# Kernel optimization log

Measured on AMD Instinct MI355X. Metric: run time of the kernel, lower is better.

Reference implementation:

```python
import jax, jax.numpy as jnp
import numpy as np

VEC_DIM = 128
NUM_DOCS = 1_000_000
NUM_WORDS = 100_000
BATCH = 16_384
K = 26  # num_noise_words + 1


def setup_inputs() -> dict:
    key = jax.random.key(0)
    k1, k2, k3, k4 = jax.random.split(key, 4)
    return {
        "context_ids": jax.random.randint(k1, (BATCH,), 0, NUM_WORDS, dtype=jnp.int32),
        "doc_ids": jax.random.randint(k2, (BATCH,), 0, NUM_DOCS, dtype=jnp.int32),
        "target_noise_ids": jax.random.randint(k3, (BATCH, K), 0, NUM_WORDS, dtype=jnp.int32),
        # learned parameters
        "D": jax.random.normal(k4, (NUM_DOCS, VEC_DIM), dtype=jnp.float32),
        "O": jnp.zeros((VEC_DIM, NUM_WORDS), dtype=jnp.float32),
    }


def reference(context_ids, doc_ids, target_noise_ids, D, O):
    # context_ids is unused in the original forward.
    d = D[doc_ids]                 # [B, V]  gather doc vectors
    w = O.T[target_noise_ids]      # [B, K, V] gather word (output) vectors
    # scores: batched dot products, equivalent to bmm(d[:,None,:], w.transpose) then squeeze
    return jnp.einsum("bv,bkv->bk", d, w)
```

## Files before the change

### kernel.cpp

```cpp
#include <hip/hip_runtime.h>

#define BATCH   16384
#define KK      26
#define VDIM    128
#define NWORDS  100000

__global__ __launch_bounds__(256) void transpose_O(const float* __restrict__ O,
                                                   float* __restrict__ Ot) {
    __shared__ float tile[VDIM][33];
    const int wbase = blockIdx.x * 32;
    const int t = threadIdx.x;

    #pragma unroll
    for (int i = 0; i < 4; ++i) {
        int idx = i * 256 + t;
        int v = idx >> 3;
        int w = (idx & 7) * 4;
        float4 r = *(const float4*)&O[(size_t)v * NWORDS + wbase + w];
        tile[v][w] = r.x; tile[v][w + 1] = r.y;
        tile[v][w + 2] = r.z; tile[v][w + 3] = r.w;
    }
    __syncthreads();

    #pragma unroll
    for (int i = 0; i < 4; ++i) {
        int idx = i * 256 + t;
        int w = idx >> 5;
        int v = (idx & 31) * 4;
        float4 r = make_float4(tile[v][w], tile[v + 1][w],
                               tile[v + 2][w], tile[v + 3][w]);
        *(float4*)&Ot[(size_t)(wbase + w) * VDIM + v] = r;
    }
}

__global__ __launch_bounds__(256) void gather_dot(const int* __restrict__ doc_ids,
                                                  const int* __restrict__ tn_ids,
                                                  const float* __restrict__ D,
                                                  const float* __restrict__ Ot,
                                                  float* __restrict__ out) {
    __shared__ float d_s[VDIM];
    const int b = blockIdx.x;

    if (threadIdx.x < VDIM) {
        const int doc = doc_ids[b];
        d_s[threadIdx.x] = D[(size_t)doc * VDIM + threadIdx.x];
    }
    __syncthreads();

    const int g = threadIdx.x >> 5;
    const int l = threadIdx.x & 31;
    const float4 dv = *(const float4*)&d_s[l * 4];

    for (int k = g; k < KK; k += 8) {
        const int word = tn_ids[b * KK + k];
        const float4 wv = *(const float4*)&Ot[(size_t)word * VDIM + l * 4];
        float p = dv.x * wv.x + dv.y * wv.y + dv.z * wv.z + dv.w * wv.w;
        #pragma unroll
        for (int off = 16; off > 0; off >>= 1)
            p += __shfl_down(p, off, 32);
        if (l == 0) out[b * KK + k] = p;
    }
}

__global__ __launch_bounds__(256) void gather_dot_direct(const int* __restrict__ doc_ids,
                                                         const int* __restrict__ tn_ids,
                                                         const float* __restrict__ D,
                                                         const float* __restrict__ O,
                                                         float* __restrict__ out) {
    __shared__ float d_s[VDIM];
    const int b = blockIdx.x;

    if (threadIdx.x < VDIM) {
        const int doc = doc_ids[b];
        d_s[threadIdx.x] = D[(size_t)doc * VDIM + threadIdx.x];
    }
    __syncthreads();

    const int wave = threadIdx.x >> 6;
    const int lane = threadIdx.x & 63;
    const int v0 = lane * 2;
    const float2 dv = *(const float2*)&d_s[v0];

    for (int k = wave; k < KK; k += 4) {
        const int word = tn_ids[b * KK + k];
        float p = dv.x * O[(size_t)v0 * NWORDS + word]
                + dv.y * O[(size_t)(v0 + 1) * NWORDS + word];
        #pragma unroll
        for (int off = 32; off > 0; off >>= 1)
            p += __shfl_down(p, off);
        if (lane == 0) out[b * KK + k] = p;
    }
}

extern "C" void kernel_launch(void* const* d_in, const int* in_sizes, int n_in,
                              void* d_out, int out_size, void* d_ws, size_t ws_size,
                              hipStream_t stream) {
    const int*   doc_ids = (const int*)d_in[1];
    const int*   tn_ids  = (const int*)d_in[2];
    const float* D       = (const float*)d_in[3];
    const float* O       = (const float*)d_in[4];
    float*       out     = (float*)d_out;

    const size_t ot_bytes = (size_t)NWORDS * VDIM * sizeof(float);

    if (ws_size >= ot_bytes) {
        float* Ot = (float*)d_ws;
        transpose_O<<<NWORDS / 32, 256, 0, stream>>>(O, Ot);
        gather_dot<<<BATCH, 256, 0, stream>>>(doc_ids, tn_ids, D, Ot, out);
    } else {
        gather_dot_direct<<<BATCH, 256, 0, stream>>>(doc_ids, tn_ids, D, O, out);
    }
}
```

Measured before the change: 620.4 us.

## Batch word-row loads, use DPP reductions, and rework transpose LDS tile

The gather kernel now reads the doc vector straight from global memory instead of staging it in shared memory, so the barrier goes away. It issues all of a group's word-row loads up front to keep more memory requests in flight, and reduces the 32-lane dot products with DPP row-shift and row-broadcast moves instead of shuffles. The transpose kernel switches to a word-major padded LDS tile, so the output phase reads one float4 per store. With a 129-float row stride, those float4 LDS reads are not 16-byte aligned for most rows, which may add access cost or depend on unaligned LDS support.

Result: no change. 615.8 us (-0.7%).

```diff
diff --git a/kernel.cpp b/kernel.cpp
--- a/kernel.cpp
+++ b/kernel.cpp
@@ -5,9 +5,16 @@
 #define VDIM    128
 #define NWORDS  100000
 
+template <int CTRL>
+__device__ __forceinline__ float dpp_mov(float x) {
+    int xi = __builtin_bit_cast(int, x);
+    int yi = __builtin_amdgcn_update_dpp(0, xi, CTRL, 0xF, 0xF, true);
+    return __builtin_bit_cast(float, yi);
+}
+
 __global__ __launch_bounds__(256) void transpose_O(const float* __restrict__ O,
                                                    float* __restrict__ Ot) {
-    __shared__ float tile[VDIM][33];
+    __shared__ float tile[32][129];
     const int wbase = blockIdx.x * 32;
     const int t = threadIdx.x;
 
@@ -15,10 +22,12 @@
     for (int i = 0; i < 4; ++i) {
         int idx = i * 256 + t;
         int v = idx >> 3;
-        int w = (idx & 7) * 4;
-        float4 r = *(const float4*)&O[(size_t)v * NWORDS + wbase + w];
-        tile[v][w] = r.x; tile[v][w + 1] = r.y;
-        tile[v][w + 2] = r.z; tile[v][w + 3] = r.w;
+        int w4 = (idx & 7) * 4;
+        float4 r = *(const float4*)&O[(size_t)v * NWORDS + wbase + w4];
+        tile[w4 + 0][v] = r.x;
+        tile[w4 + 1][v] = r.y;
+        tile[w4 + 2][v] = r.z;
+        tile[w4 + 3][v] = r.w;
     }
     __syncthreads();
 
@@ -27,9 +36,8 @@
         int idx = i * 256 + t;
         int w = idx >> 5;
         int v = (idx & 31) * 4;
-        float4 r = make_float4(tile[v][w], tile[v + 1][w],
-                               tile[v + 2][w], tile[v + 3][w]);
-        *(float4*)&Ot[(size_t)(wbase + w) * VDIM + v] = r;
+        *(float4*)&Ot[(size_t)(wbase + w) * VDIM + v] =
+            *(const float4*)&tile[w][v];
     }
 }
 
@@ -38,27 +46,42 @@
                                                   const float* __restrict__ D,
                                                   const float* __restrict__ Ot,
                                                   float* __restrict__ out) {
-    __shared__ float d_s[VDIM];
     const int b = blockIdx.x;
+    const int t = threadIdx.x;
+    const int g = t >> 5;
+    const int l = t & 31;
 
-    if (threadIdx.x < VDIM) {
-        const int doc = doc_ids[b];
-        d_s[threadIdx.x] = D[(size_t)doc * VDIM + threadIdx.x];
+    const int doc = doc_ids[b];
+    const float4 dv = *(const float4*)&D[(size_t)doc * VDIM + l * 4];
+
+    const int base = b * KK;
+    int word[4];
+    #pragma unroll
+    for (int j = 0; j < 4; ++j) {
+        int k = g + 8 * j;
+        word[j] = (k < KK) ? tn_ids[base + k] : -1;
     }
-    __syncthreads();
 
-    const int g = threadIdx.x >> 5;
-    const int l = threadIdx.x & 31;
-    const float4 dv = *(const float4*)&d_s[l * 4];
+    float4 wv[4];
+    #pragma unroll
+    for (int j = 0; j < 4; ++j) {
+        if (word[j] >= 0)
+            wv[j] = *(const float4*)&Ot[(size_t)word[j] * VDIM + l * 4];
+    }
 
-    for (int k = g; k < KK; k += 8) {
-        const int word = tn_ids[b * KK + k];
-        const float4 wv = *(const float4*)&Ot[(size_t)word * VDIM + l * 4];
-        float p = dv.x * wv.x + dv.y * wv.y + dv.z * wv.z + dv.w * wv.w;
-        #pragma unroll
-        for (int off = 16; off > 0; off >>= 1)
-            p += __shfl_down(p, off, 32);
-        if (l == 0) out[b * KK + k] = p;
+    #pragma unroll
+    for (int j = 0; j < 4; ++j) {
+        int k = g + 8 * j;
+        if (k < KK) {
+            float p = dv.x * wv[j].x + dv.y * wv[j].y
+                    + dv.z * wv[j].z + dv.w * wv[j].w;
+            p += dpp_mov<0x111>(p);
+            p += dpp_mov<0x112>(p);
+            p += dpp_mov<0x114>(p);
+            p += dpp_mov<0x118>(p);
+            p += dpp_mov<0x142>(p);
+            if (l == 31) out[base + k] = p;
+        }
     }
 }
 
```
